# Performance work log

Measured on AMD Instinct MI355X. Metric: run time of the kernel, lower is better.

## Reference

```python
import jax, jax.numpy as jnp
import numpy as np

B, S, D, H = 2, 2048, 1024, 16
DK = D // H
EPS = 1e-5


def setup_inputs() -> dict:
    key = jax.random.key(0)
    ks = jax.random.split(key, 6)
    std = (2.0 / (D + D)) ** 0.5
    return {
        "x": jax.random.normal(ks[0], (B, S, D), dtype=jnp.float32),
        "W_Q": jax.random.normal(ks[1], (D, D), dtype=jnp.float32) * std,
        "W_K": jax.random.normal(ks[2], (D, D), dtype=jnp.float32) * std,
        "W_V": jax.random.normal(ks[3], (D, D), dtype=jnp.float32) * std,
        "W_O": jax.random.normal(ks[4], (D, D), dtype=jnp.float32) * std,
        "gain": jnp.ones((D,), dtype=jnp.float32),
        "positions": jnp.arange(S, dtype=jnp.int64 if jax.config.jax_enable_x64 else jnp.int32),
        "theta": 10000,
        "max_seq_len": 2048,
    }


def rmsnorm(x, gain):
    xf = x.astype(jnp.float32)
    rms = jnp.sqrt(jnp.mean(xf * xf, axis=-1, keepdims=True) + EPS)
    return ((xf / rms) * gain).astype(x.dtype)


def apply_rope(x, sin, cos):
    # x: [..., seq, dk]; sin/cos: [seq, dk//2] broadcast over leading dims
    x_even = x[..., 0::2]
    x_odd = x[..., 1::2]
    r_even = x_even * cos - x_odd * sin
    r_odd = x_odd * cos + x_even * sin
    return jnp.stack([r_even, r_odd], axis=-1).reshape(x.shape)


def reference(x, W_Q, W_K, W_V, W_O, gain, positions, theta, max_seq_len):
    seq_len = x.shape[-2]
    Q = jnp.einsum('od,bsd->bso', W_Q, x)
    K = jnp.einsum('od,bsd->bso', W_K, x)
    V = jnp.einsum('od,bsd->bso', W_V, x)
    # RMSNorm over full d_model BEFORE head split (as in original)
    Q = rmsnorm(Q, gain)
    K = rmsnorm(K, gain)
    # split heads: [b, h, s, dk]
    Q = Q.reshape(*Q.shape[:-1], H, DK).swapaxes(-3, -2)
    K = K.reshape(*K.shape[:-1], H, DK).swapaxes(-3, -2)
    V = V.reshape(*V.shape[:-1], H, DK).swapaxes(-3, -2)
    # RoPE tables
    exponents = 2.0 * jnp.arange(DK // 2, dtype=jnp.float32) / DK
    inv_freq = 1.0 / (jnp.float32(theta) ** exponents)
    angles = positions.astype(jnp.float32)[:, None] * inv_freq[None, :]  # [S, DK//2]
    sin, cos = jnp.sin(angles), jnp.cos(angles)
    Q = apply_rope(Q, sin, cos)
    K = apply_rope(K, sin, cos)
    # causal attention
    scores = jnp.einsum('bhqd,bhkd->bhqk', Q, K) / jnp.sqrt(jnp.float32(DK))
    causal = jnp.tril(jnp.ones((seq_len, seq_len), dtype=bool))
    scores = jnp.where(causal, scores, -jnp.inf)
    attn = jax.nn.softmax(scores, axis=-1)
    out = jnp.einsum('bhqk,bhkd->bhqd', attn, V)
    out = out.swapaxes(-3, -2).reshape(*x.shape[:-1], D)
    return jnp.einsum('of,bsf->bso', W_O, out)
```

## Files before the change

kernel.cpp:

```cpp
#include <hip/hip_runtime.h>
#include <hip/hip_bf16.h>

typedef __attribute__((ext_vector_type(8))) __bf16 bf16x8;
typedef __attribute__((ext_vector_type(4))) __bf16 bf16x4;
typedef __attribute__((ext_vector_type(4))) float  f32x4;

#define S_LEN 2048
#define D_DIM 1024
#define NH    16
#define GK    1024
#define GN    1024

__device__ __forceinline__ float fast_exp2(float x) {
#if __has_builtin(__builtin_amdgcn_exp2f)
  return __builtin_amdgcn_exp2f(x);
#else
  return exp2f(x);
#endif
}

__device__ __forceinline__ void gld_lds16(const void* g, void* l) {
  __builtin_amdgcn_global_load_lds(
      (const __attribute__((address_space(1))) unsigned int*)g,
      (__attribute__((address_space(3))) unsigned int*)l, 16, 0, 0);
}

__global__ __launch_bounds__(256) void cast_all(
    const float* __restrict__ x,  const float* __restrict__ wq, const float* __restrict__ wk,
    const float* __restrict__ wv, const float* __restrict__ wo,
    __bf16* __restrict__ xb, __bf16* __restrict__ wqb, __bf16* __restrict__ wkb,
    __bf16* __restrict__ wvb, __bf16* __restrict__ wob)
{
  const int NTOT = 2 << 20;
  for (int i = blockIdx.x * 256 + threadIdx.x; i < NTOT; i += 1024 * 256) {
    const float* s; __bf16* d; int off;
    if (i < (1 << 20)) { s = x; d = xb; off = i; }
    else {
      const int j = i - (1 << 20);
      const int r = j >> 18; off = j & ((1 << 18) - 1);
      s = (r == 0) ? wq : (r == 1) ? wk : (r == 2) ? wv : wo;
      d = (r == 0) ? wqb : (r == 1) ? wkb : (r == 2) ? wvb : wob;
    }
    float4 v = ((const float4*)s)[off];
    bf16x4 o = { (__bf16)v.x, (__bf16)v.y, (__bf16)v.z, (__bf16)v.w };
    ((bf16x4*)d)[off] = o;
  }
}

__global__ __launch_bounds__(256, 6) void gemm_qkv(
    const __bf16* __restrict__ A,
    const __bf16* __restrict__ W0, const __bf16* __restrict__ W1, const __bf16* __restrict__ W2,
    __bf16* __restrict__ C0, __bf16* __restrict__ C1, __bf16* __restrict__ VtOut)
{
  const int bid = blockIdx.x;
  const int e = bid & 7, mg = e >> 1, ng = e & 1;
  const int q = bid >> 3;
  const int mode = q % 3;
  const int t = q / 3;
  const int m0 = (mg * 16 + (t & 15)) * 64;
  const int n0 = (ng * 4 + (t >> 4)) * 128;
  const __bf16* Wm = (mode == 0) ? W0 : (mode == 1) ? W1 : W2;

  __shared__ __align__(16) __bf16 As[64 * 64];
  __shared__ __align__(16) __bf16 Bs[128 * 64];

  const int tid  = threadIdx.x;
  const int lane = tid & 63;
  const int w    = tid >> 6;
  const int wr   = w >> 1, wc = w & 1;
  const int lm   = lane & 15, qd = lane >> 4;

  const __bf16* ap[2]; int loA[2];
  #pragma unroll
  for (int j = 0; j < 2; j++) {
    const int c = tid + 256 * j;
    const int r = c >> 3, cpos = c & 7;
    ap[j] = A + (size_t)(m0 + r) * GK + (cpos ^ (r & 7)) * 8;
    loA[j] = c * 8;
  }
  const __bf16* bp[4]; int loB[4];
  #pragma unroll
  for (int j = 0; j < 4; j++) {
    const int c = tid + 256 * j;
    const int r = c >> 3, cpos = c & 7;
    bp[j] = Wm + (size_t)(n0 + r) * GK + (cpos ^ (r & 7)) * 8;
    loB[j] = c * 8;
  }

  const int sw = lm & 7;

  f32x4 zero = {0.f, 0.f, 0.f, 0.f};
  f32x4 acc[2][4];
  #pragma unroll
  for (int i = 0; i < 2; i++)
    #pragma unroll
    for (int j = 0; j < 4; j++) acc[i][j] = zero;

  for (int k0 = 0; k0 < GK; k0 += 64) {
    #pragma unroll
    for (int j = 0; j < 2; j++) gld_lds16(ap[j] + k0, &As[loA[j]]);
    #pragma unroll
    for (int j = 0; j < 4; j++) gld_lds16(bp[j] + k0, &Bs[loB[j]]);
    __syncthreads();
    #pragma unroll
    for (int half = 0; half < 2; half++) {
      const int cph = ((qd + 4 * half) ^ sw) * 8;
      bf16x8 af[2], bfv[4];
      #pragma unroll
      for (int i = 0; i < 2; i++) af[i]  = *(const bf16x8*)&As[(wr * 32 + i * 16 + lm) * 64 + cph];
      #pragma unroll
      for (int j = 0; j < 4; j++) bfv[j] = *(const bf16x8*)&Bs[(wc * 64 + j * 16 + lm) * 64 + cph];
      #pragma unroll
      for (int i = 0; i < 2; i++)
        #pragma unroll
        for (int j = 0; j < 4; j++)
          acc[i][j] = __builtin_amdgcn_mfma_f32_16x16x32_bf16(af[i], bfv[j], acc[i][j], 0, 0, 0);
    }
    __syncthreads();
  }

  if (mode < 2) {
    __bf16* C = (mode == 0) ? C0 : C1;
    #pragma unroll
    for (int i = 0; i < 2; i++) {
      const int row = m0 + wr * 32 + i * 16 + qd * 4;
      #pragma unroll
      for (int j = 0; j < 4; j++) {
        const int col = n0 + wc * 64 + j * 16 + lm;
        #pragma unroll
        for (int r = 0; r < 4; r++)
          C[(size_t)(row + r) * GN + col] = (__bf16)acc[i][j][r];
      }
    }
  } else {
    #pragma unroll
    for (int i = 0; i < 2; i++) {
      const int row = m0 + wr * 32 + i * 16 + qd * 4;
      const int b = row >> 11, s = row & (S_LEN - 1);
      #pragma unroll
      for (int j = 0; j < 4; j++) {
        const int col = n0 + wc * 64 + j * 16 + lm;
        const int h = col >> 6, d = col & 63;
        bf16x4 o = { (__bf16)acc[i][j][0], (__bf16)acc[i][j][1],
                     (__bf16)acc[i][j][2], (__bf16)acc[i][j][3] };
        *(bf16x4*)(VtOut + (((size_t)(b * NH + h) * 64 + d) * S_LEN + s)) = o;
      }
    }
  }
}

__global__ __launch_bounds__(256, 6) void gemm_out64(
    const __bf16* __restrict__ A, const __bf16* __restrict__ Wm, float* __restrict__ C)
{
  const int bid = blockIdx.x;
  const int e = bid & 7, mg = e >> 1, ng = e & 1;
  const int q = bid >> 3;
  const int m0 = (mg * 16 + (q & 15)) * 64;
  const int n0 = (ng * 4 + (q >> 4)) * 128;

  __shared__ __align__(16) __bf16 As[64 * 64];
  __shared__ __align__(16) __bf16 Bs[128 * 64];

  const int tid  = threadIdx.x;
  const int lane = tid & 63;
  const int w    = tid >> 6;
  const int wr   = w >> 1, wc = w & 1;
  const int lm   = lane & 15, qd = lane >> 4;

  const __bf16* ap[2]; int loA[2];
  #pragma unroll
  for (int j = 0; j < 2; j++) {
    const int c = tid + 256 * j;
    const int r = c >> 3, cpos = c & 7;
    ap[j] = A + (size_t)(m0 + r) * GK + (cpos ^ (r & 7)) * 8;
    loA[j] = c * 8;
  }
  const __bf16* bp[4]; int loB[4];
  #pragma unroll
  for (int j = 0; j < 4; j++) {
    const int c = tid + 256 * j;
    const int r = c >> 3, cpos = c & 7;
    bp[j] = Wm + (size_t)(n0 + r) * GK + (cpos ^ (r & 7)) * 8;
    loB[j] = c * 8;
  }

  const int sw = lm & 7;

  f32x4 zero = {0.f, 0.f, 0.f, 0.f};
  f32x4 acc[2][4];
  #pragma unroll
  for (int i = 0; i < 2; i++)
    #pragma unroll
    for (int j = 0; j < 4; j++) acc[i][j] = zero;

  for (int k0 = 0; k0 < GK; k0 += 64) {
    #pragma unroll
    for (int j = 0; j < 2; j++) gld_lds16(ap[j] + k0, &As[loA[j]]);
    #pragma unroll
    for (int j = 0; j < 4; j++) gld_lds16(bp[j] + k0, &Bs[loB[j]]);
    __syncthreads();
    #pragma unroll
    for (int half = 0; half < 2; half++) {
      const int cph = ((qd + 4 * half) ^ sw) * 8;
      bf16x8 af[2], bfv[4];
      #pragma unroll
      for (int i = 0; i < 2; i++) af[i]  = *(const bf16x8*)&As[(wr * 32 + i * 16 + lm) * 64 + cph];
      #pragma unroll
      for (int j = 0; j < 4; j++) bfv[j] = *(const bf16x8*)&Bs[(wc * 64 + j * 16 + lm) * 64 + cph];
      #pragma unroll
      for (int i = 0; i < 2; i++)
        #pragma unroll
        for (int j = 0; j < 4; j++)
          acc[i][j] = __builtin_amdgcn_mfma_f32_16x16x32_bf16(af[i], bfv[j], acc[i][j], 0, 0, 0);
    }
    __syncthreads();
  }

  #pragma unroll
  for (int i = 0; i < 2; i++) {
    const int row = m0 + wr * 32 + i * 16 + qd * 4;
    #pragma unroll
    for (int j = 0; j < 4; j++) {
      const int col = n0 + wc * 64 + j * 16 + lm;
      #pragma unroll
      for (int r = 0; r < 4; r++)
        C[(size_t)(row + r) * GN + col] = acc[i][j][r];
    }
  }
}

__global__ __launch_bounds__(256) void norm_rope(
    const __bf16* __restrict__ Qf, const __bf16* __restrict__ Kf,
    const float* __restrict__ gain, const int* __restrict__ positions,
    const int* __restrict__ theta_p,
    __bf16* __restrict__ Qh, __bf16* __restrict__ Kh)
{
  const int row = blockIdx.x;
  const int s = row & (S_LEN - 1), b = row >> 11;
  const int t = threadIdx.x, d0 = t * 4;

  const bf16x4 qv = *(const bf16x4*)(Qf + (size_t)row * D_DIM + d0);
  const bf16x4 kv = *(const bf16x4*)(Kf + (size_t)row * D_DIM + d0);
  const float q0 = (float)qv[0], q1 = (float)qv[1], q2 = (float)qv[2], q3 = (float)qv[3];
  const float k0 = (float)kv[0], k1 = (float)kv[1], k2 = (float)kv[2], k3 = (float)kv[3];

  float sq = q0 * q0 + q1 * q1 + q2 * q2 + q3 * q3;
  float sk = k0 * k0 + k1 * k1 + k2 * k2 + k3 * k3;
  #pragma unroll
  for (int off = 32; off; off >>= 1) { sq += __shfl_xor(sq, off); sk += __shfl_xor(sk, off); }
  __shared__ float red[8];
  const int lane = t & 63, wv = t >> 6;
  if (lane == 0) { red[wv] = sq; red[4 + wv] = sk; }
  __syncthreads();
  sq = red[0] + red[1] + red[2] + red[3];
  sk = red[4] + red[5] + red[6] + red[7];
  const float SC2 = 0.125f * 1.44269504089f;
  const float invq = rsqrtf(sq * (1.0f / 1024.0f) + 1e-5f) * SC2;
  const float invk = rsqrtf(sk * (1.0f / 1024.0f) + 1e-5f);

  const float4 g = *(const float4*)(gain + d0);
  const float qn0 = q0 * invq * g.x, qn1 = q1 * invq * g.y;
  const float qn2 = q2 * invq * g.z, qn3 = q3 * invq * g.w;
  const float kn0 = k0 * invk * g.x, kn1 = k1 * invk * g.y;
  const float kn2 = k2 * invk * g.z, kn3 = k3 * invk * g.w;

  const float pos = (float)positions[s];
  const float th  = (float)theta_p[0];
  const int idx = d0 & 63, h = d0 >> 6, p0 = idx >> 1;
  const float lg32 = __log2f(th) * (1.0f / 32.0f);
  const float f0 = fast_exp2(-(float)p0 * lg32);
  const float f1 = fast_exp2(-(float)(p0 + 1) * lg32);
  float s0, cc0, s1, cc1;
  __sincosf(pos * f0, &s0, &cc0);
  __sincosf(pos * f1, &s1, &cc1);

  const float qe0 = qn0 * cc0 - qn1 * s0, qo0 = qn1 * cc0 + qn0 * s0;
  const float qe1 = qn2 * cc1 - qn3 * s1, qo1 = qn3 * cc1 + qn2 * s1;
  const float ke0 = kn0 * cc0 - kn1 * s0, ko0 = kn1 * cc0 + kn0 * s0;
  const float ke1 = kn2 * cc1 - kn3 * s1, ko1 = kn3 * cc1 + kn2 * s1;

  const size_t obase = ((size_t)((b * NH + h) * S_LEN + s)) * 64 + idx;
  bf16x4 qo = { (__bf16)qe0, (__bf16)qo0, (__bf16)qe1, (__bf16)qo1 };
  bf16x4 ko = { (__bf16)ke0, (__bf16)ko0, (__bf16)ke1, (__bf16)ko1 };
  *(bf16x4*)(Qh + obase) = qo;
  *(bf16x4*)(Kh + obase) = ko;
}

__global__ __launch_bounds__(256) void attn_fwd(
    const __bf16* __restrict__ Qh, const __bf16* __restrict__ Kh,
    const __bf16* __restrict__ Vt, __bf16* __restrict__ Ob)
{
  const int bid = blockIdx.x;
  const int g   = bid >> 5, gj = g & 7, gs = g >> 3;
  const int qt  = (gs == 0) ? 31 - gj : (gs == 1) ? gj : (gs == 2) ? 23 - gj : 8 + gj;
  const int rr  = bid & 31;
  const int bh  = (rr & 7) * 4 + (rr >> 3);
  const int tid = threadIdx.x, lane = tid & 63, w = tid >> 6;
  const int lm = lane & 15, qd = lane >> 4;

  __shared__ __align__(16) __bf16 smem[8192 + 8192 + 4096];
  __bf16* Ks = smem;
  __bf16* Vs = smem + 8192;
  __bf16* Pw = smem + 16384 + w * 1024;

  const int row0 = qt * 64 + w * 16;
  const size_t qbase = (size_t)bh * S_LEN * 64;
  const bf16x8 aq0 = *(const bf16x8*)(Qh + qbase + (size_t)(row0 + lm) * 64 + qd * 8);
  const bf16x8 aq1 = *(const bf16x8*)(Qh + qbase + (size_t)(row0 + lm) * 64 + 32 + qd * 8);

  const __bf16* Kb = Kh + (size_t)bh * S_LEN * 64;
  const __bf16* Vb = Vt + (size_t)bh * 64 * S_LEN;
  const int c0 = tid, c1 = 256 + tid;
  const int kr0 = c0 >> 3, kr1 = c1 >> 3;
  const int kg0 = ((c0 & 7) ^ (kr0 & 7)) * 8;
  const int kg1 = ((c1 & 7) ^ (kr1 & 7)) * 8;
  const int cpA = (qd ^ (lm & 7)) * 8;
  const int cpB = cpA ^ 32;

  auto stage = [&](int buf, int k0) {
    __bf16* Kd = Ks + buf * 4096;
    __bf16* Vd = Vs + buf * 4096;
    gld_lds16(Kb + (size_t)(k0 + kr0) * 64 + kg0, &Kd[c0 * 8]);
    gld_lds16(Kb + (size_t)(k0 + kr1) * 64 + kg1, &Kd[c1 * 8]);
    gld_lds16(Vb + (size_t)kr0 * S_LEN + k0 + kg0, &Vd[c0 * 8]);
    gld_lds16(Vb + (size_t)kr1 * S_LEN + k0 + kg1, &Vd[c1 * 8]);
  };

  f32x4 zero = {0.f, 0.f, 0.f, 0.f};
  f32x4 lacc = zero;
  f32x4 o[4];
  #pragma unroll
  for (int jb = 0; jb < 4; jb++) o[jb] = zero;

  bf16x8 ones;
  #pragma unroll
  for (int i = 0; i < 8; i++) ones[i] = (__bf16)1.0f;

  stage(0, 0);

  const int rowg = row0 + qd * 4;
  const int pxor = qd * 4;

  for (int kt = 0; kt <= qt; ++kt) {
    const int cur = kt & 1;
    __syncthreads();
    if (kt < qt) stage(cur ^ 1, (kt + 1) * 64);

    const __bf16* Kc = Ks + cur * 4096;
    const __bf16* Vc = Vs + cur * 4096;
    const int k0 = kt * 64;

    float p[4][4];
    const bool diag = (kt == qt);
    #pragma unroll
    for (int kb = 0; kb < 4; kb++) {
      const int krow = (kb * 16 + lm) * 64;
      const bf16x8 bk0 = *(const bf16x8*)&Kc[krow + cpA];
      const bf16x8 bk1 = *(const bf16x8*)&Kc[krow + cpB];
      f32x4 sc = zero;
      sc = __builtin_amdgcn_mfma_f32_16x16x32_bf16(aq0, bk0, sc, 0, 0, 0);
      sc = __builtin_amdgcn_mfma_f32_16x16x32_bf16(aq1, bk1, sc, 0, 0, 0);
      if (diag) {
        const int colg = k0 + kb * 16 + lm;
        #pragma unroll
        for (int r = 0; r < 4; r++)
          p[kb][r] = (colg <= rowg + r) ? fast_exp2(sc[r]) : 0.f;
      } else {
        #pragma unroll
        for (int r = 0; r < 4; r++) p[kb][r] = fast_exp2(sc[r]);
      }
    }

    #pragma unroll
    for (int kb = 0; kb < 4; kb++) {
      const int cb = kb * 2 + (lm >> 3), wi = lm & 7;
      #pragma unroll
      for (int r = 0; r < 4; r++) {
        const int prow = pxor + r;
        Pw[prow * 64 + ((cb ^ (prow & 7)) << 3) + wi] = (__bf16)p[kb][r];
      }
    }

    const bf16x8 ap0 = *(const bf16x8*)&Pw[lm * 64 + cpA];
    const bf16x8 ap1 = *(const bf16x8*)&Pw[lm * 64 + cpB];
    lacc = __builtin_amdgcn_mfma_f32_16x16x32_bf16(ap1, ones,
           __builtin_amdgcn_mfma_f32_16x16x32_bf16(ap0, ones, lacc, 0, 0, 0), 0, 0, 0);
    #pragma unroll
    for (int jb = 0; jb < 4; jb++) {
      const int vrow = (jb * 16 + lm) * 64;
      const bf16x8 bv0 = *(const bf16x8*)&Vc[vrow + cpA];
      const bf16x8 bv1 = *(const bf16x8*)&Vc[vrow + cpB];
      o[jb] = __builtin_amdgcn_mfma_f32_16x16x32_bf16(ap1, bv1,
              __builtin_amdgcn_mfma_f32_16x16x32_bf16(ap0, bv0, o[jb], 0, 0, 0), 0, 0, 0);
    }
  }

  const int b = bh >> 4, h = bh & 15;
  #pragma unroll
  for (int r = 0; r < 4; r++) {
    const float inv = 1.0f / lacc[r];
    const size_t base = ((size_t)(b * S_LEN + rowg + r)) * D_DIM + h * 64;
    #pragma unroll
    for (int jb = 0; jb < 4; jb++)
      Ob[base + jb * 16 + lm] = (__bf16)(o[jb][r] * inv);
  }
}

extern "C" void kernel_launch(void* const* d_in, const int* in_sizes, int n_in,
                              void* d_out, int out_size, void* d_ws, size_t ws_size,
                              hipStream_t stream)
{
  (void)in_sizes; (void)n_in; (void)out_size; (void)ws_size;
  const float* x    = (const float*)d_in[0];
  const float* WQ   = (const float*)d_in[1];
  const float* WK   = (const float*)d_in[2];
  const float* WV   = (const float*)d_in[3];
  const float* WO   = (const float*)d_in[4];
  const float* gain = (const float*)d_in[5];
  const int* positions = (const int*)d_in[6];
  const int* theta     = (const int*)d_in[7];
  float* out = (float*)d_out;

  char* ws = (char*)d_ws;
  const size_t MB = 1024 * 1024;
  __bf16* xb  = (__bf16*)(ws + 0);
  __bf16* WQb = (__bf16*)(ws + 8  * MB);
  __bf16* WKb = (__bf16*)(ws + 10 * MB);
  __bf16* WVb = (__bf16*)(ws + 12 * MB);
  __bf16* WOb = (__bf16*)(ws + 14 * MB);
  __bf16* Qfb = (__bf16*)(ws + 16 * MB);
  __bf16* Kfb = (__bf16*)(ws + 24 * MB);
  __bf16* Vt  = (__bf16*)(ws + 32 * MB);
  __bf16* Qh  = (__bf16*)(ws + 40 * MB);
  __bf16* Kh  = (__bf16*)(ws + 48 * MB);
  __bf16* Ob  = (__bf16*)(ws + 56 * MB);

  cast_all<<<1024, 256, 0, stream>>>(x, WQ, WK, WV, WO, xb, WQb, WKb, WVb, WOb);
  gemm_qkv<<<1536, 256, 0, stream>>>(xb, WQb, WKb, WVb, Qfb, Kfb, Vt);
  norm_rope<<<4096, 256, 0, stream>>>(Qfb, Kfb, gain, positions, theta, Qh, Kh);
  attn_fwd<<<1024, 256, 0, stream>>>(Qh, Kh, Vt, Ob);
  gemm_out64<<<512, 256, 0, stream>>>(Ob, WOb, out);
}
```

Baseline: 179.8 us.

## Keep attention P in registers via transposed score MFMA, drop LDS round-trip

```diff
diff --git a/kernel.cpp b/kernel.cpp
--- a/kernel.cpp
+++ b/kernel.cpp
@@ -4,6 +4,7 @@
 typedef __attribute__((ext_vector_type(8))) __bf16 bf16x8;
 typedef __attribute__((ext_vector_type(4))) __bf16 bf16x4;
 typedef __attribute__((ext_vector_type(4))) float  f32x4;
+typedef __attribute__((ext_vector_type(4))) short  s16x4;
 
 #define S_LEN 2048
 #define D_DIM 1024
@@ -16,6 +17,15 @@
   return __builtin_amdgcn_exp2f(x);
 #else
   return exp2f(x);
+#endif
+}
+
+__device__ __forceinline__ f32x4 mfma16(bf16x4 a, bf16x4 b, f32x4 c) {
+#if __has_builtin(__builtin_amdgcn_mfma_f32_16x16x16_bf16)
+  return __builtin_amdgcn_mfma_f32_16x16x16_bf16(a, b, c, 0, 0, 0);
+#else
+  return __builtin_amdgcn_mfma_f32_16x16x16bf16_1k(
+      __builtin_bit_cast(s16x4, a), __builtin_bit_cast(s16x4, b), c, 0, 0, 0);
 #endif
 }
 
@@ -298,15 +308,15 @@
   const int tid = threadIdx.x, lane = tid & 63, w = tid >> 6;
   const int lm = lane & 15, qd = lane >> 4;
 
-  __shared__ __align__(16) __bf16 smem[8192 + 8192 + 4096];
+  __shared__ __align__(16) __bf16 smem[8192 + 8192];
   __bf16* Ks = smem;
   __bf16* Vs = smem + 8192;
-  __bf16* Pw = smem + 16384 + w * 1024;
 
   const int row0 = qt * 64 + w * 16;
+  const int qglob = row0 + lm;
   const size_t qbase = (size_t)bh * S_LEN * 64;
-  const bf16x8 aq0 = *(const bf16x8*)(Qh + qbase + (size_t)(row0 + lm) * 64 + qd * 8);
-  const bf16x8 aq1 = *(const bf16x8*)(Qh + qbase + (size_t)(row0 + lm) * 64 + 32 + qd * 8);
+  const bf16x8 aq0 = *(const bf16x8*)(Qh + qbase + (size_t)qglob * 64 + qd * 8);
+  const bf16x8 aq1 = *(const bf16x8*)(Qh + qbase + (size_t)qglob * 64 + 32 + qd * 8);
 
   const __bf16* Kb = Kh + (size_t)bh * S_LEN * 64;
   const __bf16* Vb = Vt + (size_t)bh * 64 * S_LEN;
@@ -332,14 +342,11 @@
   #pragma unroll
   for (int jb = 0; jb < 4; jb++) o[jb] = zero;
 
-  bf16x8 ones;
-  #pragma unroll
-  for (int i = 0; i < 8; i++) ones[i] = (__bf16)1.0f;
+  bf16x4 ones4;
+  #pragma unroll
+  for (int i = 0; i < 4; i++) ones4[i] = (__bf16)1.0f;
 
   stage(0, 0);
-
-  const int rowg = row0 + qd * 4;
-  const int pxor = qd * 4;
 
   for (int kt = 0; kt <= qt; ++kt) {
     const int cur = kt & 1;
@@ -349,60 +356,53 @@
     const __bf16* Kc = Ks + cur * 4096;
     const __bf16* Vc = Vs + cur * 4096;
     const int k0 = kt * 64;
-
-    float p[4][4];
     const bool diag = (kt == qt);
+
+    bf16x4 pfrag[4];
     #pragma unroll
     for (int kb = 0; kb < 4; kb++) {
       const int krow = (kb * 16 + lm) * 64;
-      const bf16x8 bk0 = *(const bf16x8*)&Kc[krow + cpA];
-      const bf16x8 bk1 = *(const bf16x8*)&Kc[krow + cpB];
+      const bf16x8 ak0 = *(const bf16x8*)&Kc[krow + cpA];
+      const bf16x8 ak1 = *(const bf16x8*)&Kc[krow + cpB];
       f32x4 sc = zero;
-      sc = __builtin_amdgcn_mfma_f32_16x16x32_bf16(aq0, bk0, sc, 0, 0, 0);
-      sc = __builtin_amdgcn_mfma_f32_16x16x32_bf16(aq1, bk1, sc, 0, 0, 0);
+      sc = __builtin_amdgcn_mfma_f32_16x16x32_bf16(ak0, aq0, sc, 0, 0, 0);
+      sc = __builtin_amdgcn_mfma_f32_16x16x32_bf16(ak1, aq1, sc, 0, 0, 0);
+      float p[4];
       if (diag) {
-        const int colg = k0 + kb * 16 + lm;
+        const int keyb = k0 + kb * 16 + qd * 4;
         #pragma unroll
         for (int r = 0; r < 4; r++)
-          p[kb][r] = (colg <= rowg + r) ? fast_exp2(sc[r]) : 0.f;
+          p[r] = (keyb + r <= qglob) ? fast_exp2(sc[r]) : 0.f;
       } else {
         #pragma unroll
-        for (int r = 0; r < 4; r++) p[kb][r] = fast_exp2(sc[r]);
+        for (int r = 0; r < 4; r++) p[r] = fast_exp2(sc[r]);
       }
-    }
-
-    #pragma unroll
-    for (int kb = 0; kb < 4; kb++) {
-      const int cb = kb * 2 + (lm >> 3), wi = lm & 7;
-      #pragma unroll
-      for (int r = 0; r < 4; r++) {
-        const int prow = pxor + r;
-        Pw[prow * 64 + ((cb ^ (prow & 7)) << 3) + wi] = (__bf16)p[kb][r];
+      bf16x4 pf = { (__bf16)p[0], (__bf16)p[1], (__bf16)p[2], (__bf16)p[3] };
+      pfrag[kb] = pf;
+      lacc = mfma16(ones4, pf, lacc);
+    }
+
+    #pragma unroll
+    for (int jb = 0; jb < 4; jb++) {
+      const int vrow = jb * 16 + lm;
+      const int rsw = vrow & 7;
+      #pragma unroll
+      for (int kb = 0; kb < 4; kb++) {
+        const int c = 2 * kb + (qd >> 1);
+        const bf16x4 av = *(const bf16x4*)&Vc[vrow * 64 + ((c ^ rsw) << 3) + (qd & 1) * 4];
+        o[jb] = mfma16(av, pfrag[kb], o[jb]);
       }
     }
-
-    const bf16x8 ap0 = *(const bf16x8*)&Pw[lm * 64 + cpA];
-    const bf16x8 ap1 = *(const bf16x8*)&Pw[lm * 64 + cpB];
-    lacc = __builtin_amdgcn_mfma_f32_16x16x32_bf16(ap1, ones,
-           __builtin_amdgcn_mfma_f32_16x16x32_bf16(ap0, ones, lacc, 0, 0, 0), 0, 0, 0);
-    #pragma unroll
-    for (int jb = 0; jb < 4; jb++) {
-      const int vrow = (jb * 16 + lm) * 64;
-      const bf16x8 bv0 = *(const bf16x8*)&Vc[vrow + cpA];
-      const bf16x8 bv1 = *(const bf16x8*)&Vc[vrow + cpB];
-      o[jb] = __builtin_amdgcn_mfma_f32_16x16x32_bf16(ap1, bv1,
-              __builtin_amdgcn_mfma_f32_16x16x32_bf16(ap0, bv0, o[jb], 0, 0, 0), 0, 0, 0);
-    }
   }
 
   const int b = bh >> 4, h = bh & 15;
-  #pragma unroll
-  for (int r = 0; r < 4; r++) {
-    const float inv = 1.0f / lacc[r];
-    const size_t base = ((size_t)(b * S_LEN + rowg + r)) * D_DIM + h * 64;
-    #pragma unroll
-    for (int jb = 0; jb < 4; jb++)
-      Ob[base + jb * 16 + lm] = (__bf16)(o[jb][r] * inv);
+  const float inv = 1.0f / lacc[0];
+  const size_t base = ((size_t)(b * S_LEN + qglob)) * D_DIM + h * 64 + qd * 4;
+  #pragma unroll
+  for (int jb = 0; jb < 4; jb++) {
+    bf16x4 ov = { (__bf16)(o[jb][0] * inv), (__bf16)(o[jb][1] * inv),
+                  (__bf16)(o[jb][2] * inv), (__bf16)(o[jb][3] * inv) };
+    *(bf16x4*)(Ob + base + jb * 16) = ov;
   }
 }
 
```

Result: faster. 175.1 us (-2.6%).
